# Performance work log

Hardware: AMD Instinct MI355X
Metric: run time of the kernel (lower is better)

Reference implementation:

```python
import jax, jax.numpy as jnp
import numpy as np

NEG = -1e9  # sentinel for suppressed / below-threshold scores
SCORE_THRESHOLD = 0.05
IOU_THRESHOLD = 0.5
MAX_DETECTIONS = 100


def _iou_one_vs_all(box, boxes):
    # box: (4,) in (x1, y1, x2, y2); boxes: (N, 4)
    ix1 = jnp.maximum(box[0], boxes[:, 0])
    iy1 = jnp.maximum(box[1], boxes[:, 1])
    ix2 = jnp.minimum(box[2], boxes[:, 2])
    iy2 = jnp.minimum(box[3], boxes[:, 3])
    inter = jnp.maximum(ix2 - ix1, 0.0) * jnp.maximum(iy2 - iy1, 0.0)
    a1 = (box[2] - box[0]) * (box[3] - box[1])
    a2 = (boxes[:, 2] - boxes[:, 0]) * (boxes[:, 3] - boxes[:, 1])
    return inter / jnp.maximum(a1 + a2 - inter, 1e-8)


def _nms_single_class(boxes, scores):
    # boxes: (N, 4), scores: (N,). Fixed-shape greedy NMS via scan.
    scores0 = jnp.where(scores > SCORE_THRESHOLD, scores, NEG)

    def step(s, _):
        best = jnp.argmax(s)
        bscore = s[best]
        bbox = boxes[best]
        iou = _iou_one_vs_all(bbox, boxes)
        # suppress overlapping boxes (incl. the selected one, IoU=1)
        s_next = jnp.where(iou > IOU_THRESHOLD, NEG, s)
        return s_next, (bscore, bbox)

    _, (keep_scores, keep_boxes) = jax.lax.scan(step, scores0, None, length=MAX_DETECTIONS)
    return keep_scores, keep_boxes  # (M,), (M, 4)


def _filter_one_image(boxes, classification):
    # boxes: (N, 4), classification: (N, C)
    C = classification.shape[1]
    cls_scores = classification.T  # (C, N)
    ks, kb = jax.vmap(lambda s: _nms_single_class(boxes, s))(cls_scores)  # (C, M), (C, M, 4)
    labels = jnp.broadcast_to(jnp.arange(C, dtype=jnp.int32)[:, None], ks.shape)
    scores_flat = ks.reshape(-1)          # (C*M,)
    boxes_flat = kb.reshape(-1, 4)        # (C*M, 4)
    labels_flat = labels.reshape(-1)      # (C*M,)
    top_scores, top_idx = jax.lax.top_k(scores_flat, MAX_DETECTIONS)
    top_boxes = boxes_flat[top_idx]
    top_labels = labels_flat[top_idx]
    valid = top_scores > SCORE_THRESHOLD
    out_scores = jnp.where(valid, top_scores, -1.0)
    out_boxes = jnp.where(valid[:, None], top_boxes, -1.0)
    out_labels = jnp.where(valid, top_labels, -1).astype(jnp.int32)
    return out_boxes, out_scores, out_labels


def setup_inputs() -> dict:
    key = jax.random.key(0)
    k1, k2, k3 = jax.random.split(key, 3)
    B, N, C = 2, 10000, 80
    xy = jax.random.uniform(k1, (B, N, 2), dtype=jnp.float32) * 900.0
    wh = jax.random.uniform(k2, (B, N, 2), dtype=jnp.float32) * 100.0 + 1.0
    boxes = jnp.concatenate([xy, xy + wh], axis=-1)  # valid (x1,y1,x2,y2)
    # raise to 4th power so most scores fall below the 0.05 threshold (realistic)
    classification = jax.random.uniform(k3, (B, N, C), dtype=jnp.float32) ** 4
    return {"boxes": boxes, "classification": classification}


@jax.jit
def reference(boxes, classification):
    # boxes: (B, N, 4), classification: (B, N, C)
    out_boxes, out_scores, out_labels = jax.vmap(_filter_one_image)(boxes, classification)
    return out_boxes, out_scores, out_labels
```

## Files before the change

### kernel.cpp

```cpp
#include <hip/hip_runtime.h>
#include <float.h>
#include <stdint.h>

#pragma clang fp contract(off)

typedef unsigned long long ull;

#define NEGV   (-1e9f)
#define THRV   (0.05f)
#define MAXDET 100
#define NB     1152
#define BKBASE 31385
#define SLABSZ 1024
#define CHTGT  512
#define TKCAP  1024
#define BT     512

__device__ __forceinline__ int bktOf(unsigned u) {
  int v = (int)(u >> 15) - BKBASE;
  return v < 0 ? 0 : (v > NB - 1 ? NB - 1 : v);
}

__device__ __forceinline__ bool killpair(
    float qx1, float qy1, float qx2, float qy2, float qa,
    float x1, float y1, float x2, float y2, float a)
{
  const float iw = fminf(qx2, x2) - fmaxf(qx1, x1);
  const float ih = fminf(qy2, y2) - fmaxf(qy1, y1);
  if (iw <= 0.f || ih <= 0.f) return false;
  const float inter = iw * ih;
  const float den = fmaxf((qa + a) - inter, 1e-8f);
  const float i2 = inter + inter;
  if (i2 > den * 1.00001f) return true;
  if (i2 < den * 0.99999f) return false;
  return (inter / den) > 0.5f;
}

__device__ __forceinline__ int suffix_scan(int* hist, int* wtot,
                                           int tid, int lane, int wid) {
  int c0 = 0, c1 = 0, c2 = 0;
  if (tid < NB / 3) {
    c0 = hist[NB - 1 - 3 * tid];
    c1 = hist[NB - 2 - 3 * tid];
    c2 = hist[NB - 3 - 3 * tid];
  }
  const int tsum = c0 + c1 + c2;
  int inc = tsum;
#pragma unroll
  for (int off = 1; off < 64; off <<= 1) {
    const int u = __shfl_up(inc, off, 64);
    if (lane >= off) inc += u;
  }
  if (lane == 63) wtot[wid] = inc;
  __syncthreads();
  int wbase = 0, tot = 0;
#pragma unroll
  for (int w = 0; w < BT / 64; ++w) {
    const int v = wtot[w];
    if (w < wid) wbase += v;
    tot += v;
  }
  const int excl = wbase + inc - tsum;
  if (tid < NB / 3) {
    hist[NB - 1 - 3 * tid] = excl;
    hist[NB - 2 - 3 * tid] = excl + c0;
    hist[NB - 3 - 3 * tid] = excl + c0 + c1;
  }
  __syncthreads();
  return tot;
}

__device__ int run_scan(const ull* keys, int cn,
                        const float4* __restrict__ bb4,
                        const float4* boxPre, int preN,
                        float4* kboxS, float* kscoreS, float* kareaS,
                        ull* wkill, ull* killby,
                        int tid, int lane, int wid)
{
#pragma clang fp contract(off)
  constexpr int NW = BT / 64;
  constexpr int CPW = 64 / NW;
  int nk = 0;
  for (int base = 0; base < cn && nk < MAXDET; base += 64) {
    const int nc = min(64, cn - base);
    const bool valid = lane < nc;
    const int p = base + lane;
    ull key = 0ull;
    if (valid) key = keys[p];
    const float score = __uint_as_float((unsigned)(key >> 32));
    const int idx = (int)(~(unsigned)key);
    float4 bx = make_float4(0.f, 0.f, 0.f, 0.f);
    if (valid) bx = (p < preN) ? boxPre[p] : bb4[idx];
    const float area = (bx.z - bx.x) * (bx.w - bx.y);

    bool kill = false;
    for (int e = wid; e < nk; e += NW) {
      const float4 q = kboxS[e];
      kill = kill || killpair(q.x, q.y, q.z, q.w, kareaS[e],
                              bx.x, bx.y, bx.z, bx.w, area);
    }
    {
      const ull bm = __ballot(valid && kill);
      if (lane == 0) wkill[wid] = bm;
    }
    {
      const int cb = wid * CPW;
#pragma unroll
      for (int jj = 0; jj < CPW; ++jj) {
        const int j = cb + jj;
        if (j < nc) {
          const float jx1 = __int_as_float(__builtin_amdgcn_readlane(__float_as_int(bx.x), j));
          const float jy1 = __int_as_float(__builtin_amdgcn_readlane(__float_as_int(bx.y), j));
          const float jx2 = __int_as_float(__builtin_amdgcn_readlane(__float_as_int(bx.z), j));
          const float jy2 = __int_as_float(__builtin_amdgcn_readlane(__float_as_int(bx.w), j));
          const float ja  = __int_as_float(__builtin_amdgcn_readlane(__float_as_int(area), j));
          const bool kij = valid && killpair(jx1, jy1, jx2, jy2, ja,
                                             bx.x, bx.y, bx.z, bx.w, area);
          const ull bm = __ballot(kij);
          if (lane == 0) killby[j] = bm;
        }
      }
    }
    __syncthreads();

    ull kmask = 0;
#pragma unroll
    for (int w = 0; w < NW; ++w) kmask |= wkill[w];
    ull alive = ~kmask;
    alive &= (nc >= 64) ? ~0ull : ((1ull << nc) - 1ull);
    const ull kb = killby[lane];
    for (int j = 0; j < 64; ++j) {
      if ((alive >> j) & 1ull) {
        const unsigned klo = (unsigned)__builtin_amdgcn_readlane((int)(unsigned)kb, j);
        const unsigned khi = (unsigned)__builtin_amdgcn_readlane((int)(unsigned)(kb >> 32), j);
        const ull km = ((ull)khi << 32) | klo;
        alive &= ~(km & ((~1ull) << j));
      }
    }
    if (wid == 0) {
      const int rank = (int)__popcll(alive & ((1ull << lane) - 1ull));
      if (((alive >> lane) & 1ull) && (nk + rank < MAXDET)) {
        kboxS[nk + rank] = bx;
        kscoreS[nk + rank] = score;
        kareaS[nk + rank] = area;
      }
    }
    nk += min((int)__popcll(alive), MAXDET - nk);
    __syncthreads();
  }
  return nk;
}

__device__ int selection_tail(const float* __restrict__ col, int N, int C,
                              ull lastKey, int nk,
                              const float4* __restrict__ bb4,
                              float4* kboxS, float* kscoreS, float* kareaS,
                              ull* redS, int* flagS,
                              int tid, int lane, int wid)
{
#pragma clang fp contract(off)
  while (nk < MAXDET) {
    ull best = 0ull;
    for (int i = tid; i < N; i += BT) {
      const float s = col[(size_t)i * C];
      if (s > THRV) {
        const ull k = ((ull)__float_as_uint(s) << 32) | (unsigned)(~i);
        if (k < lastKey && k > best) best = k;
      }
    }
#pragma unroll
    for (int off = 32; off >= 1; off >>= 1) {
      const ull o = __shfl_xor(best, off, 64);
      if (o > best) best = o;
    }
    if (lane == 0) redS[wid] = best;
    if (tid == 0) *flagS = 0;
    __syncthreads();
    ull gbest = redS[0];
#pragma unroll
    for (int w = 1; w < BT / 64; ++w) if (redS[w] > gbest) gbest = redS[w];
    if (gbest == 0ull) break;
    const int idx = (int)(~(unsigned)gbest);
    const float4 q = bb4[idx];
    const float qa = (q.z - q.x) * (q.w - q.y);
    bool kl = false;
    for (int e = tid; e < nk; e += BT) {
      const float4 kq = kboxS[e];
      kl = kl || killpair(kq.x, kq.y, kq.z, kq.w, kareaS[e],
                          q.x, q.y, q.z, q.w, qa);
    }
    if (kl) atomicOr(flagS, 1);
    __syncthreads();
    const bool killed = (*flagS != 0);
    if (!killed) {
      if (tid == 0) {
        kboxS[nk] = q;
        kscoreS[nk] = __uint_as_float((unsigned)(gbest >> 32));
        kareaS[nk] = qa;
      }
      ++nk;
    }
    __syncthreads();
    lastKey = gbest;
  }
  return nk;
}

__device__ __forceinline__ unsigned agent_load_u32(const float* p) {
  return __hip_atomic_load((const unsigned*)p, __ATOMIC_RELAXED,
                           __HIP_MEMORY_SCOPE_AGENT);
}

__global__ __launch_bounds__(BT, 1) void nms_fused(
    const float* __restrict__ boxes, const float* __restrict__ cls,
    float* __restrict__ ksc, float* __restrict__ kbx,
    ull* __restrict__ gcand, unsigned* __restrict__ done,
    float* __restrict__ out, int N, int C, int B)
{
#pragma clang fp contract(off)
  const int bc = blockIdx.x;
  const int b = bc / C, c = bc % C;
  const int tid = threadIdx.x, lane = tid & 63, wid = tid >> 6;
  const float* col = cls + (size_t)b * N * C + c;
  const float4* bb4 = (const float4*)(boxes + (size_t)b * N * 4);

  __shared__ int hist[NB];
  __shared__ int wtot[BT / 64];
  __shared__ ull slab[SLABSZ];
  __shared__ ull sorted[SLABSZ];
  __shared__ float4 boxPre[SLABSZ];
  __shared__ float4 kboxS[MAXDET];
  __shared__ float kscoreS[MAXDET], kareaS[MAXDET];
  __shared__ ull wkill[BT / 64], killby[64], redS[BT / 64];
  __shared__ int flagS, bkLoS, tBs, cposS, lastS;

  for (int i = tid; i < NB; i += BT) hist[i] = 0;
  if (tid == 0) bkLoS = -1;
  __syncthreads();
  for (int i = tid; i < N; i += BT) {
    const float s = col[(size_t)i * C];
    if (s > THRV) atomicAdd(&hist[bktOf(__float_as_uint(s))], 1);
  }
  __syncthreads();
  const int cn = suffix_scan(hist, wtot, tid, lane, wid);
  for (int bk = tid; bk < NB; bk += BT)
    if (hist[bk] >= CHTGT) atomicMax(&bkLoS, bk);
  __syncthreads();
  const int bkLo = bkLoS;
  const int chunkCnt = (bkLo >= 0) ? hist[bkLo] : cn;

  int nk = 0;
  if (cn > 0) {
    if (chunkCnt <= SLABSZ) {
      for (int i = tid; i < N; i += BT) {
        const float s = col[(size_t)i * C];
        if (s > THRV) {
          const unsigned u = __float_as_uint(s);
          const int bk = bktOf(u);
          if (bk > bkLo)
            slab[atomicAdd(&hist[bk], 1)] = ((ull)u << 32) | (unsigned)(~i);
        }
      }
      __syncthreads();
      for (int e = tid; e < chunkCnt; e += BT) {
        const ull k = slab[e];
        int r = 0;
        for (int j = 0; j < chunkCnt; ++j) r += (slab[j] > k) ? 1 : 0;
        sorted[r] = k;
      }
      __syncthreads();
      for (int e = tid; e < chunkCnt; e += BT)
        boxPre[e] = bb4[(int)(~(unsigned)sorted[e])];
      __syncthreads();
      nk = run_scan(sorted, chunkCnt, bb4, boxPre, chunkCnt,
                    kboxS, kscoreS, kareaS, wkill, killby, tid, lane, wid);
      if (nk < MAXDET && chunkCnt < cn)
        nk = selection_tail(col, N, C, sorted[chunkCnt - 1], nk, bb4,
                            kboxS, kscoreS, kareaS, redS, &flagS,
                            tid, lane, wid);
    } else {
      nk = selection_tail(col, N, C, ~0ull, 0, bb4,
                          kboxS, kscoreS, kareaS, redS, &flagS,
                          tid, lane, wid);
    }
  }

  float* ko  = ksc + (size_t)bc * MAXDET;
  float* kbo = kbx + (size_t)bc * MAXDET * 4;
  for (int e = tid; e < MAXDET; e += BT) {
    if (e < nk) {
      const float4 q = kboxS[e];
      ko[e] = kscoreS[e];
      kbo[e * 4 + 0] = q.x; kbo[e * 4 + 1] = q.y;
      kbo[e * 4 + 2] = q.z; kbo[e * 4 + 3] = q.w;
    } else {
      ko[e] = NEGV;
      kbo[e * 4 + 0] = 0.f; kbo[e * 4 + 1] = 0.f;
      kbo[e * 4 + 2] = 0.f; kbo[e * 4 + 3] = 0.f;
    }
  }

  __threadfence();
  __syncthreads();
  if (tid == 0) {
    const unsigned old = __hip_atomic_fetch_add(
        &done[b], 1u, __ATOMIC_ACQ_REL, __HIP_MEMORY_SCOPE_AGENT);
    lastS = (old == (unsigned)(C - 1)) ? 1 : 0;
  }
  __syncthreads();
  if (!lastS) return;

  const int T = C * MAXDET;
  const float* s0 = ksc + (size_t)b * T;
  ull* gc = gcand + (size_t)b * T;
  float* ob = out;
  float* os = out + (size_t)B * MAXDET * 4;
  float* ol = os + (size_t)B * MAXDET;

  for (int i = tid; i < NB; i += BT) hist[i] = 0;
  if (tid == 0) { cposS = 0; tBs = 0; }
  __syncthreads();
  for (int f = tid; f < T; f += BT) {
    const unsigned u = agent_load_u32(&s0[f]);
    if (__uint_as_float(u) > THRV) atomicAdd(&hist[bktOf(u)], 1);
  }
  __syncthreads();
  suffix_scan(hist, wtot, tid, lane, wid);
  for (int bk = tid; bk < NB; bk += BT)
    if (hist[bk] < MAXDET && (bk == 0 || hist[bk - 1] >= MAXDET)) tBs = bk;
  __syncthreads();
  const int t = tBs;
  for (int f = tid; f < T; f += BT) {
    const unsigned u = agent_load_u32(&s0[f]);
    if (__uint_as_float(u) > THRV && bktOf(u) >= t) {
      const int p = atomicAdd(&cposS, 1);
      const ull key = ((ull)u << 32) | (unsigned)(~f);
      if (p < TKCAP) sorted[p] = key; else gc[p] = key;
    }
  }
  __syncthreads();
  const int nc = cposS;
  const int nw = min(nc, MAXDET);
  for (int s2 = nw + tid; s2 < MAXDET; s2 += BT) {
    float* od = ob + ((size_t)b * MAXDET + s2) * 4;
    od[0] = -1.f; od[1] = -1.f; od[2] = -1.f; od[3] = -1.f;
    os[(size_t)b * MAXDET + s2] = -1.f;
    ol[(size_t)b * MAXDET + s2] = -1.f;
  }
  for (int e = tid; e < nc; e += BT) {
    const ull k = (e < TKCAP) ? sorted[e] : gc[e];
    int rank = 0;
    for (int j = 0; j < nc; ++j) {
      const ull o = (j < TKCAP) ? sorted[j] : gc[j];
      rank += (o > k) ? 1 : 0;
    }
    if (rank < MAXDET) {
      const int f = (int)(~(unsigned)k);
      const float sc = __uint_as_float((unsigned)(k >> 32));
      const float* bp = kbx + ((size_t)b * T + f) * 4;
      float* od = ob + ((size_t)b * MAXDET + rank) * 4;
      od[0] = __uint_as_float(agent_load_u32(&bp[0]));
      od[1] = __uint_as_float(agent_load_u32(&bp[1]));
      od[2] = __uint_as_float(agent_load_u32(&bp[2]));
      od[3] = __uint_as_float(agent_load_u32(&bp[3]));
      os[(size_t)b * MAXDET + rank] = sc;
      ol[(size_t)b * MAXDET + rank] = (float)(f / MAXDET);
    }
  }
}

extern "C" void kernel_launch(void* const* d_in, const int* in_sizes, int n_in,
                              void* d_out, int out_size, void* d_ws, size_t ws_size,
                              hipStream_t stream) {
  const float* boxes = (const float*)d_in[0];
  const float* cls   = (const float*)d_in[1];
  const int B = out_size / (MAXDET * 6);
  const int N = in_sizes[0] / (B * 4);
  const int C = in_sizes[1] / (B * N);

  char* ws = (char*)d_ws;
  ull* gcand = (ull*)ws;   ws += (size_t)B * C * MAXDET * 8;
  float* kbx = (float*)ws; ws += (size_t)B * C * MAXDET * 16;
  float* ksc = (float*)ws; ws += (size_t)B * C * MAXDET * 4;
  unsigned* done = (unsigned*)ws;

  hipMemsetAsync(done, 0, (size_t)B * 4, stream);
  nms_fused<<<dim3(B * C), dim3(BT), 0, stream>>>(
      boxes, cls, ksc, kbx, gcand, done, (float*)d_out, N, C, B);
}
```

Baseline: 169.2 us.

## Transpose class scores in-kernel with grid barrier for contiguous per-class reads

Adds a prologue phase where all blocks cooperatively transpose the (N,C) classification tensor into a (C,N) workspace through a shared-memory tile, followed by a software grid-wide barrier on an atomic counter. Per-class histogram, slab-fill and selection-tail passes then read contiguous memory, using float4 loads where aligned, instead of strided reads with stride C. This removes the uncoalesced column access that each of the 160 blocks repeats over several passes. In exchange it adds a full extra read and write of the score tensor, plus a spin barrier that assumes all blocks are co-resident (guarded by gridDim <= 256). It also simplifies run_scan to read only preloaded boxes.

```diff
diff --git a/kernel.cpp b/kernel.cpp
--- a/kernel.cpp
+++ b/kernel.cpp
@@ -71,8 +71,7 @@
 }
 
 __device__ int run_scan(const ull* keys, int cn,
-                        const float4* __restrict__ bb4,
-                        const float4* boxPre, int preN,
+                        const float4* boxPre,
                         float4* kboxS, float* kscoreS, float* kareaS,
                         ull* wkill, ull* killby,
                         int tid, int lane, int wid)
@@ -88,9 +87,8 @@
     ull key = 0ull;
     if (valid) key = keys[p];
     const float score = __uint_as_float((unsigned)(key >> 32));
-    const int idx = (int)(~(unsigned)key);
     float4 bx = make_float4(0.f, 0.f, 0.f, 0.f);
-    if (valid) bx = (p < preN) ? boxPre[p] : bb4[idx];
+    if (valid) bx = boxPre[p];
     const float area = (bx.z - bx.x) * (bx.w - bx.y);
 
     bool kill = false;
@@ -151,7 +149,7 @@
   return nk;
 }
 
-__device__ int selection_tail(const float* __restrict__ col, int N, int C,
+__device__ int selection_tail(const float* __restrict__ col, int N, int stride,
                               ull lastKey, int nk,
                               const float4* __restrict__ bb4,
                               float4* kboxS, float* kscoreS, float* kareaS,
@@ -162,7 +160,7 @@
   while (nk < MAXDET) {
     ull best = 0ull;
     for (int i = tid; i < N; i += BT) {
-      const float s = col[(size_t)i * C];
+      const float s = col[(size_t)i * stride];
       if (s > THRV) {
         const ull k = ((ull)__float_as_uint(s) << 32) | (unsigned)(~i);
         if (k < lastKey && k > best) best = k;
@@ -213,17 +211,17 @@
 
 __global__ __launch_bounds__(BT, 1) void nms_fused(
     const float* __restrict__ boxes, const float* __restrict__ cls,
-    float* __restrict__ ksc, float* __restrict__ kbx,
-    ull* __restrict__ gcand, unsigned* __restrict__ done,
+    float* __restrict__ clsT, float* __restrict__ ksc, float* __restrict__ kbx,
+    ull* __restrict__ gcand, unsigned* __restrict__ ctrs,
     float* __restrict__ out, int N, int C, int B)
 {
 #pragma clang fp contract(off)
   const int bc = blockIdx.x;
   const int b = bc / C, c = bc % C;
   const int tid = threadIdx.x, lane = tid & 63, wid = tid >> 6;
-  const float* col = cls + (size_t)b * N * C + c;
   const float4* bb4 = (const float4*)(boxes + (size_t)b * N * 4);
 
+  __shared__ float tile[32][33];
   __shared__ int hist[NB];
   __shared__ int wtot[BT / 64];
   __shared__ ull slab[SLABSZ];
@@ -234,12 +232,68 @@
   __shared__ ull wkill[BT / 64], killby[64], redS[BT / 64];
   __shared__ int flagS, bkLoS, tBs, cposS, lastS;
 
+  const bool useT = (gridDim.x <= 256);
+  if (useT) {
+    const int ntC = (C + 31) / 32, ntN = (N + 31) / 32;
+    const int ntot = B * ntN * ntC;
+    const int tx = tid & 31, ty = tid >> 5;
+    for (int t = blockIdx.x; t < ntot; t += gridDim.x) {
+      const int ct = t % ntC;
+      const int nt = (t / ntC) % ntN;
+      const int tb = t / (ntC * ntN);
+#pragma unroll
+      for (int r = ty; r < 32; r += 16) {
+        const int n = nt * 32 + r, cc = ct * 32 + tx;
+        if (n < N && cc < C) tile[r][tx] = cls[((size_t)tb * N + n) * C + cc];
+      }
+      __syncthreads();
+#pragma unroll
+      for (int r = ty; r < 32; r += 16) {
+        const int cc = ct * 32 + r, n = nt * 32 + tx;
+        if (n < N && cc < C) clsT[((size_t)tb * C + cc) * N + n] = tile[tx][r];
+      }
+      __syncthreads();
+    }
+    __threadfence();
+    __syncthreads();
+    if (tid == 0) {
+      __hip_atomic_fetch_add(&ctrs[0], 1u, __ATOMIC_ACQ_REL,
+                             __HIP_MEMORY_SCOPE_AGENT);
+      while (__hip_atomic_load(&ctrs[0], __ATOMIC_ACQUIRE,
+                               __HIP_MEMORY_SCOPE_AGENT) < gridDim.x)
+        __builtin_amdgcn_s_sleep(2);
+    }
+    __syncthreads();
+    __threadfence();
+  }
+
+  const float* colS = useT ? (clsT + (size_t)bc * N)
+                           : (cls + (size_t)b * N * C + c);
+  const int stride = useT ? 1 : C;
+  const bool vec4 = (stride == 1) && ((((size_t)colS) & 15) == 0);
+  const int nv4 = vec4 ? (N >> 2) : 0;
+  const float4* col4 = (const float4*)colS;
+
   for (int i = tid; i < NB; i += BT) hist[i] = 0;
   if (tid == 0) bkLoS = -1;
   __syncthreads();
-  for (int i = tid; i < N; i += BT) {
-    const float s = col[(size_t)i * C];
-    if (s > THRV) atomicAdd(&hist[bktOf(__float_as_uint(s))], 1);
+  if (vec4) {
+    for (int i = tid; i < nv4; i += BT) {
+      const float4 v = col4[i];
+      if (v.x > THRV) atomicAdd(&hist[bktOf(__float_as_uint(v.x))], 1);
+      if (v.y > THRV) atomicAdd(&hist[bktOf(__float_as_uint(v.y))], 1);
+      if (v.z > THRV) atomicAdd(&hist[bktOf(__float_as_uint(v.z))], 1);
+      if (v.w > THRV) atomicAdd(&hist[bktOf(__float_as_uint(v.w))], 1);
+    }
+    for (int i = (nv4 << 2) + tid; i < N; i += BT) {
+      const float s = colS[i];
+      if (s > THRV) atomicAdd(&hist[bktOf(__float_as_uint(s))], 1);
+    }
+  } else {
+    for (int i = tid; i < N; i += BT) {
+      const float s = colS[(size_t)i * stride];
+      if (s > THRV) atomicAdd(&hist[bktOf(__float_as_uint(s))], 1);
+    }
   }
   __syncthreads();
   const int cn = suffix_scan(hist, wtot, tid, lane, wid);
@@ -252,13 +306,39 @@
   int nk = 0;
   if (cn > 0) {
     if (chunkCnt <= SLABSZ) {
-      for (int i = tid; i < N; i += BT) {
-        const float s = col[(size_t)i * C];
-        if (s > THRV) {
-          const unsigned u = __float_as_uint(s);
-          const int bk = bktOf(u);
-          if (bk > bkLo)
-            slab[atomicAdd(&hist[bk], 1)] = ((ull)u << 32) | (unsigned)(~i);
+      if (vec4) {
+        for (int i = tid; i < nv4; i += BT) {
+          const float4 v = col4[i];
+          const float sv[4] = {v.x, v.y, v.z, v.w};
+#pragma unroll
+          for (int j = 0; j < 4; ++j) {
+            if (sv[j] > THRV) {
+              const unsigned u = __float_as_uint(sv[j]);
+              const int bk = bktOf(u);
+              if (bk > bkLo)
+                slab[atomicAdd(&hist[bk], 1)] =
+                    ((ull)u << 32) | (unsigned)(~(4 * i + j));
+            }
+          }
+        }
+        for (int i = (nv4 << 2) + tid; i < N; i += BT) {
+          const float s = colS[i];
+          if (s > THRV) {
+            const unsigned u = __float_as_uint(s);
+            const int bk = bktOf(u);
+            if (bk > bkLo)
+              slab[atomicAdd(&hist[bk], 1)] = ((ull)u << 32) | (unsigned)(~i);
+          }
+        }
+      } else {
+        for (int i = tid; i < N; i += BT) {
+          const float s = colS[(size_t)i * stride];
+          if (s > THRV) {
+            const unsigned u = __float_as_uint(s);
+            const int bk = bktOf(u);
+            if (bk > bkLo)
+              slab[atomicAdd(&hist[bk], 1)] = ((ull)u << 32) | (unsigned)(~i);
+          }
         }
       }
       __syncthreads();
@@ -272,14 +352,14 @@
       for (int e = tid; e < chunkCnt; e += BT)
         boxPre[e] = bb4[(int)(~(unsigned)sorted[e])];
       __syncthreads();
-      nk = run_scan(sorted, chunkCnt, bb4, boxPre, chunkCnt,
+      nk = run_scan(sorted, chunkCnt, boxPre,
                     kboxS, kscoreS, kareaS, wkill, killby, tid, lane, wid);
       if (nk < MAXDET && chunkCnt < cn)
-        nk = selection_tail(col, N, C, sorted[chunkCnt - 1], nk, bb4,
+        nk = selection_tail(colS, N, stride, sorted[chunkCnt - 1], nk, bb4,
                             kboxS, kscoreS, kareaS, redS, &flagS,
                             tid, lane, wid);
     } else {
-      nk = selection_tail(col, N, C, ~0ull, 0, bb4,
+      nk = selection_tail(colS, N, stride, ~0ull, 0, bb4,
                           kboxS, kscoreS, kareaS, redS, &flagS,
                           tid, lane, wid);
     }
@@ -304,7 +384,7 @@
   __syncthreads();
   if (tid == 0) {
     const unsigned old = __hip_atomic_fetch_add(
-        &done[b], 1u, __ATOMIC_ACQ_REL, __HIP_MEMORY_SCOPE_AGENT);
+        &ctrs[1 + b], 1u, __ATOMIC_ACQ_REL, __HIP_MEMORY_SCOPE_AGENT);
     lastS = (old == (unsigned)(C - 1)) ? 1 : 0;
   }
   __syncthreads();
@@ -379,12 +459,13 @@
   const int C = in_sizes[1] / (B * N);
 
   char* ws = (char*)d_ws;
-  ull* gcand = (ull*)ws;   ws += (size_t)B * C * MAXDET * 8;
-  float* kbx = (float*)ws; ws += (size_t)B * C * MAXDET * 16;
-  float* ksc = (float*)ws; ws += (size_t)B * C * MAXDET * 4;
-  unsigned* done = (unsigned*)ws;
-
-  hipMemsetAsync(done, 0, (size_t)B * 4, stream);
+  float* clsT = (float*)ws; ws += (size_t)B * C * N * 4;
+  ull* gcand = (ull*)ws;    ws += (size_t)B * C * MAXDET * 8;
+  float* kbx = (float*)ws;  ws += (size_t)B * C * MAXDET * 16;
+  float* ksc = (float*)ws;  ws += (size_t)B * C * MAXDET * 4;
+  unsigned* ctrs = (unsigned*)ws;
+
+  hipMemsetAsync(ctrs, 0, (size_t)(1 + B) * 4, stream);
   nms_fused<<<dim3(B * C), dim3(BT), 0, stream>>>(
-      boxes, cls, ksc, kbx, gcand, done, (float*)d_out, N, C, B);
-}
+      boxes, cls, clsT, ksc, kbx, gcand, ctrs, (float*)d_out, N, C, B);
+}
```

Result: slower. 209.1 us (+23.6%).
